# Kernel optimization log

Hardware: AMD Instinct MI355X
Metric: run time of the kernel (lower is better)

Reference implementation:

```python
import jax, jax.numpy as jnp
import numpy as np


def _lstm(x, Wih, Whh, bih, bhh):
    # x: [T,B,E] -> outputs [T,B,H]; torch gate order i,f,g,o
    B = x.shape[1]
    H = Whh.shape[1]
    bias = bih + bhh
    def step(carry, xt):
        h, c = carry
        g = xt @ Wih.T + h @ Whh.T + bias  # [B,4H]
        i, f, gg, o = jnp.split(g, 4, axis=-1)
        c = jax.nn.sigmoid(f) * c + jax.nn.sigmoid(i) * jnp.tanh(gg)
        h = jax.nn.sigmoid(o) * jnp.tanh(c)
        return (h, c), h
    init = (jnp.zeros((B, H), x.dtype), jnp.zeros((B, H), x.dtype))
    _, hs = jax.lax.scan(step, init, x)
    return hs


def setup_inputs():
    key = jax.random.key(0)
    ks = jax.random.split(key, 16)
    B, T, V, NT, E, H = 128, 512, 50000, 24, 128, 256
    Hd = H // 2  # per-direction hidden
    s = 0.08
    x = jax.random.randint(ks[0], (B, T), 0, V)
    tags = jax.random.randint(ks[1], (B, T), 0, NT)
    lengths = jax.random.randint(ks[2], (B,), T // 2, T + 1)
    mask = jnp.arange(T)[None, :] < lengths[:, None]  # [B,T] bool, position 0 always valid
    emb = (jax.random.normal(ks[3], (V, E)) * s).at[0].set(0.0)  # padding_idx=0 row zeroed
    Wih_f = jax.random.normal(ks[4], (4 * Hd, E)) * s
    Whh_f = jax.random.normal(ks[5], (4 * Hd, Hd)) * s
    bih_f = jax.random.normal(ks[6], (4 * Hd,)) * s
    bhh_f = jax.random.normal(ks[7], (4 * Hd,)) * s
    Wih_b = jax.random.normal(ks[8], (4 * Hd, E)) * s
    Whh_b = jax.random.normal(ks[9], (4 * Hd, Hd)) * s
    bih_b = jax.random.normal(ks[10], (4 * Hd,)) * s
    bhh_b = jax.random.normal(ks[11], (4 * Hd,)) * s
    W_out = jax.random.normal(ks[12], (NT, H)) * s
    b_out = jnp.zeros((NT,))
    transitions = jax.random.normal(ks[13], (NT, NT))
    start_trans = jax.random.normal(ks[14], (NT,))
    end_trans = jax.random.normal(ks[15], (NT,))
    return {"x": x, "tags": tags, "mask": mask, "emb": emb,
            "Wih_f": Wih_f, "Whh_f": Whh_f, "bih_f": bih_f, "bhh_f": bhh_f,
            "Wih_b": Wih_b, "Whh_b": Whh_b, "bih_b": bih_b, "bhh_b": bhh_b,
            "W_out": W_out, "b_out": b_out, "transitions": transitions,
            "start_trans": start_trans, "end_trans": end_trans}


def reference(x, tags, mask, emb, Wih_f, Whh_f, bih_f, bhh_f,
              Wih_b, Whh_b, bih_b, bhh_b, W_out, b_out,
              transitions, start_trans, end_trans):
    # --- emissions (dropout is identity in eval) ---
    xe = emb[x]                       # [B,T,E]
    xt = xe.transpose(1, 0, 2)        # [T,B,E]
    hf = _lstm(xt, Wih_f, Whh_f, bih_f, bhh_f)               # [T,B,Hd]
    hb = _lstm(xt[::-1], Wih_b, Whh_b, bih_b, bhh_b)[::-1]   # [T,B,Hd]
    h = jnp.concatenate([hf, hb], axis=-1).transpose(1, 0, 2)  # [B,T,H]
    emissions = h @ W_out.T + b_out   # [B,T,NT]

    # --- CRF forward algorithm (logZ) via scan over time ---
    score0 = start_trans + emissions[:, 0]  # [B,NT]
    em_rest = emissions[:, 1:].transpose(1, 0, 2)  # [T-1,B,NT]
    m_rest = mask[:, 1:].T                        # [T-1,B]
    def fwd_step(score, inp):
        em_t, m_t = inp
        ns = jax.nn.logsumexp(score[:, :, None] + transitions[None] + em_t[:, None, :], axis=1)
        return jnp.where(m_t[:, None], ns, score), None
    score, _ = jax.lax.scan(fwd_step, score0, (em_rest, m_rest))
    logZ = jax.nn.logsumexp(score + end_trans, axis=1)  # [B]

    # --- gold path score, fully vectorized ---
    mf = mask.astype(emissions.dtype)
    emit = jnp.take_along_axis(emissions, tags[:, :, None], axis=2)[:, :, 0]  # [B,T]
    trans = transitions[tags[:, :-1], tags[:, 1:]]                            # [B,T-1]
    gold = start_trans[tags[:, 0]] + emit[:, 0] + jnp.sum((trans + emit[:, 1:]) * mf[:, 1:], axis=1)
    last_idx = mask.sum(axis=1) - 1
    last_tags = jnp.take_along_axis(tags, last_idx[:, None], axis=1)[:, 0]
    gold = gold + end_trans[last_tags]

    return jnp.mean(logZ - gold)
```

## Files before the change

kernel.cpp:

```cpp
#include <hip/hip_runtime.h>
#include <hip/hip_bf16.h>

typedef unsigned short u16;
typedef unsigned int   u32;
typedef _Float16 half2_t __attribute__((ext_vector_type(2)));
typedef short    bf16x8 __attribute__((ext_vector_type(8)));
typedef float    f32x4  __attribute__((ext_vector_type(4)));
typedef u32      u32x4v __attribute__((ext_vector_type(4)));

#define TT   512

__device__ __forceinline__ float sigf(float x)  { return 1.0f / (1.0f + __expf(-x)); }
__device__ __forceinline__ float tanhf_(float x){ return 1.0f - 2.0f / (__expf(2.0f * x) + 1.0f); }

__device__ __forceinline__ u16 f2bf(float x) {
  __hip_bfloat16 h = __float2bfloat16(x);
  return *reinterpret_cast<u16*>(&h);
}
__device__ __forceinline__ float bf2f(u16 u) { return __uint_as_float(((u32)u) << 16); }
__device__ __forceinline__ u32 pk2(float a, float b) {
  return (u32)f2bf(a) | ((u32)f2bf(b) << 16);
}
__device__ __forceinline__ u16 f2h(float x) {
  _Float16 h = (_Float16)x;
  union { _Float16 f; u16 u; } c; c.f = h; return c.u;
}
__device__ __forceinline__ half2_t u2h2(u32 v) {
  union { u32 u; half2_t h; } c; c.u = v; return c.h;
}

__global__ __launch_bounds__(256) void prep_k(
    const float* __restrict__ Wih_f, const float* __restrict__ Wih_b,
    const float* __restrict__ Whh_f, const float* __restrict__ Whh_b,
    const float* __restrict__ bih_f, const float* __restrict__ bhh_f,
    const float* __restrict__ bih_b, const float* __restrict__ bhh_b,
    const float* __restrict__ W_out,
    u16* __restrict__ Wb, u32* __restrict__ Whh16, float* __restrict__ bias,
    u32* __restrict__ Wout16)
{
  int i = blockIdx.x * 256 + threadIdx.x;
  {
    int n = i >> 7, k = i & 127;
    float v = (n < 512) ? Wih_f[n * 128 + k] : Wih_b[(n - 512) * 128 + k];
    Wb[i] = f2bf(v);
  }
  if (i < 65536) {
    int d = i >> 15, rem = i & 32767, r = rem >> 6, kp = rem & 63;
    const float* W = d ? Whh_b : Whh_f;
    float f0 = W[r * 128 + 2 * kp], f1 = W[r * 128 + 2 * kp + 1];
    Whh16[i] = (u32)f2h(f0) | ((u32)f2h(f1) << 16);
  }
  if (i < 1024) {
    int d = i >> 9, jj = i & 511;
    bias[i] = d ? (bih_b[jj] + bhh_b[jj]) : (bih_f[jj] + bhh_f[jj]);
  }
  if (i < 3072) {
    Wout16[i] = (u32)f2h(W_out[2 * i]) | ((u32)f2h(W_out[2 * i + 1]) << 16);
  }
}

__global__ __launch_bounds__(256) void embed_k(
    const int* __restrict__ x, const float* __restrict__ emb, u16* __restrict__ xe)
{
  const int tid = threadIdx.x;
  const int r = blockIdx.x * 8 + (tid >> 5);
  const int lane = tid & 31;
  int token = x[r];
  float4 v = *(const float4*)&emb[(size_t)token * 128 + lane * 4];
  uint2 p; p.x = pk2(v.x, v.y); p.y = pk2(v.z, v.w);
  *(uint2*)&xe[(size_t)r * 128 + lane * 4] = p;
}

__global__ __launch_bounds__(256, 2) void gates_mfma_k(
    const u16* __restrict__ xe, const u16* __restrict__ Wb,
    const float* __restrict__ bias, u16* __restrict__ Gout)
{
  const int tid = threadIdx.x;
  const int wid = tid >> 6, l = tid & 63;
  const int wm = wid >> 1, wn = wid & 1;
  const int M0 = blockIdx.y * 128, N0 = blockIdx.x * 128;
  const int lr = l & 15, lk = l >> 4;

  f32x4 acc[4][4];
#pragma unroll
  for (int i = 0; i < 4; ++i)
#pragma unroll
    for (int j = 0; j < 4; ++j) acc[i][j] = (f32x4){0.f, 0.f, 0.f, 0.f};

#pragma unroll
  for (int ks = 0; ks < 4; ++ks) {
    bf16x8 a[4], b[4];
#pragma unroll
    for (int mi = 0; mi < 4; ++mi)
      a[mi] = *(const bf16x8*)&xe[(size_t)(M0 + wm * 64 + mi * 16 + lr) * 128 + ks * 32 + lk * 8];
#pragma unroll
    for (int ni = 0; ni < 4; ++ni)
      b[ni] = *(const bf16x8*)&Wb[(size_t)(N0 + wn * 64 + ni * 16 + lr) * 128 + ks * 32 + lk * 8];
#pragma unroll
    for (int mi = 0; mi < 4; ++mi)
#pragma unroll
      for (int ni = 0; ni < 4; ++ni)
        acc[mi][ni] = __builtin_amdgcn_mfma_f32_16x16x32_bf16(a[mi], b[ni], acc[mi][ni], 0, 0, 0);
  }

  float bcol[4];
#pragma unroll
  for (int ni = 0; ni < 4; ++ni) bcol[ni] = bias[N0 + wn * 64 + ni * 16 + lr];

  __shared__ u16 cs[128][136];
#pragma unroll
  for (int mi = 0; mi < 4; ++mi)
#pragma unroll
    for (int ni = 0; ni < 4; ++ni) {
      int col = wn * 64 + ni * 16 + lr;
#pragma unroll
      for (int r = 0; r < 4; ++r) {
        int row = wm * 64 + mi * 16 + lk * 4 + r;
        cs[row][col] = f2bf(acc[mi][ni][r] + bcol[ni]);
      }
    }
  __syncthreads();
  {
    int row = tid >> 1, c0 = (tid & 1) * 64;
    u16* dst = &Gout[(size_t)(M0 + row) * 1024 + N0 + c0];
#pragma unroll
    for (int q = 0; q < 8; ++q)
      *(uint4*)&dst[q * 8] = *(const uint4*)&cs[row][c0 + q * 8];
  }
}

__global__ __launch_bounds__(256, 1) void lstm_k(
    const u16* __restrict__ G, const u32* __restrict__ Whh16,
    u16* __restrict__ Hout)
{
  const int bid = blockIdx.x;
  const int dir = bid >> 7, b = bid & 127;
  const int tid = threadIdx.x;
  const int r   = tid & 127;
  const int hi  = tid >> 7;
  const int g0  = r + hi * 256;
  const int g1  = g0 + 128;

  const u32* w0p = Whh16 + ((size_t)dir << 15) + (size_t)g0 * 64;
  const u32* w1p = Whh16 + ((size_t)dir << 15) + (size_t)g1 * 64;

#define LDQ(n) u32x4v q##n = *(const u32x4v*)(w0p + 4*(n)); \
               u32x4v p##n = *(const u32x4v*)(w1p + 4*(n));
  LDQ(0)  LDQ(1)  LDQ(2)  LDQ(3)  LDQ(4)  LDQ(5)  LDQ(6)  LDQ(7)
  LDQ(8)  LDQ(9)  LDQ(10) LDQ(11) LDQ(12) LDQ(13) LDQ(14) LDQ(15)
#undef LDQ
#define PIN(a,b,c,d) asm volatile("" : "+v"(a), "+v"(b), "+v"(c), "+v"(d));
  PIN(q0,q1,q2,q3)   PIN(q4,q5,q6,q7)   PIN(q8,q9,q10,q11)   PIN(q12,q13,q14,q15)
  PIN(p0,p1,p2,p3)   PIN(p4,p5,p6,p7)   PIN(p8,p9,p10,p11)   PIN(p12,p13,p14,p15)
#undef PIN

  __shared__ __align__(16) u32 hs2[64];
  __shared__ float gact[512];
  if (tid < 64) hs2[tid] = 0u;
  float c = 0.0f;
  __syncthreads();

  const u16* gp = G + (size_t)b * TT * 1024 + (size_t)dir * 512;
  int t = dir ? (TT - 1) : 0;
  const int ts = dir ? -1 : 1;
  u16 gb0 = gp[(size_t)t * 1024 + g0];
  u16 gb1 = gp[(size_t)t * 1024 + g1];

  for (int step = 0; step < TT; ++step) {
    float gpre0 = bf2f(gb0), gpre1 = bf2f(gb1);
    if (step < TT - 1) {
      gb0 = gp[(size_t)(t + ts) * 1024 + g0];
      gb1 = gp[(size_t)(t + ts) * 1024 + g1];
    }

    float a00 = 0.f, a01 = 0.f, a10 = 0.f, a11 = 0.f;
    const u32x4v* h4 = (const u32x4v*)hs2;
#define DOT(n) { u32x4v hv = h4[n]; \
    a00 = __builtin_amdgcn_fdot2(u2h2(hv.x), u2h2(q##n.x), a00, false); \
    a00 = __builtin_amdgcn_fdot2(u2h2(hv.y), u2h2(q##n.y), a00, false); \
    a01 = __builtin_amdgcn_fdot2(u2h2(hv.z), u2h2(q##n.z), a01, false); \
    a01 = __builtin_amdgcn_fdot2(u2h2(hv.w), u2h2(q##n.w), a01, false); \
    a10 = __builtin_amdgcn_fdot2(u2h2(hv.x), u2h2(p##n.x), a10, false); \
    a10 = __builtin_amdgcn_fdot2(u2h2(hv.y), u2h2(p##n.y), a10, false); \
    a11 = __builtin_amdgcn_fdot2(u2h2(hv.z), u2h2(p##n.z), a11, false); \
    a11 = __builtin_amdgcn_fdot2(u2h2(hv.w), u2h2(p##n.w), a11, false); }
    DOT(0)  DOT(1)  DOT(2)  DOT(3)  DOT(4)  DOT(5)  DOT(6)  DOT(7)
    DOT(8)  DOT(9)  DOT(10) DOT(11) DOT(12) DOT(13) DOT(14) DOT(15)
#undef DOT
    float v0 = gpre0 + a00 + a01;
    float v1 = gpre1 + a10 + a11;

    float act0, act1;
    if (hi == 0) { act0 = sigf(v0);   act1 = sigf(v1); }
    else         { act0 = tanhf_(v0); act1 = sigf(v1); }
    gact[g0] = act0; gact[g1] = act1;
    __syncthreads();
    if (hi == 0) {
      float iv = gact[r], fv = gact[128 + r], gv = gact[256 + r], ov = gact[384 + r];
      c = fv * c + iv * gv;
      float hvv = ov * tanhf_(c);
      ((u16*)hs2)[r] = f2h(hvv);
      Hout[((size_t)(b * TT + t)) * 256 + dir * 128 + r] = f2h(hvv);
    }
    __syncthreads();
    t += ts;
  }
}

__global__ __launch_bounds__(256) void emis_k(
    const u16* __restrict__ Hb, const u32* __restrict__ Wout16,
    const float* __restrict__ b_out, float* __restrict__ em)
{
  __shared__ __align__(16) u32 wl2[24 * 128];
  __shared__ float bo[24];
  const int tid = threadIdx.x;
  for (int i = tid; i < 3072; i += 256) wl2[i] = Wout16[i];
  if (tid < 24) bo[tid] = b_out[tid];
  __syncthreads();

  const int m = blockIdx.x * 256 + tid;
  float acc[24];
#pragma unroll
  for (int tg = 0; tg < 24; ++tg) acc[tg] = bo[tg];

  const u32* h2 = (const u32*)(Hb + (size_t)m * 256);
  for (int ck = 0; ck < 16; ++ck) {
    uint4 hv = *(const uint4*)(h2 + ck * 4);
#pragma unroll
    for (int tg = 0; tg < 24; ++tg) {
      u32x4v wv = *(const u32x4v*)&wl2[tg * 128 + ck * 4];
      float a = acc[tg];
      a = __builtin_amdgcn_fdot2(u2h2(hv.x), u2h2(wv.x), a, false);
      a = __builtin_amdgcn_fdot2(u2h2(hv.y), u2h2(wv.y), a, false);
      a = __builtin_amdgcn_fdot2(u2h2(hv.z), u2h2(wv.z), a, false);
      a = __builtin_amdgcn_fdot2(u2h2(hv.w), u2h2(wv.w), a, false);
      acc[tg] = a;
    }
  }
#pragma unroll
  for (int t6 = 0; t6 < 6; ++t6) {
    float4 o;
    o.x = acc[t6*4+0]; o.y = acc[t6*4+1]; o.z = acc[t6*4+2]; o.w = acc[t6*4+3];
    *(float4*)&em[(size_t)m * 24 + t6 * 4] = o;
  }
}

__device__ __forceinline__ int get_mask(const void* mp, int idx, bool byte_mode) {
  return byte_mode ? (int)((const unsigned char*)mp)[idx] : ((const int*)mp)[idx];
}

__global__ __launch_bounds__(64) void crf_k(
    const float* __restrict__ em, const int* __restrict__ tags,
    const void* __restrict__ maskp, const float* __restrict__ trans,
    const float* __restrict__ start_tr, const float* __restrict__ end_tr,
    float* __restrict__ out)
{
  const int b = blockIdx.x;
  const int tid = threadIdx.x;
  __shared__ float tr[24 * 24];
  __shared__ float scs[24];
  for (int i = tid; i < 24 * 24; i += 64) tr[i] = trans[i];
  const bool byte_mode = (*(const u32*)maskp != 1u);

  int cnt = 0;
  for (int t = tid; t < TT; t += 64) cnt += get_mask(maskp, b * TT + t, byte_mode);
#pragma unroll
  for (int off = 32; off > 0; off >>= 1) cnt += __shfl_down(cnt, off);
  cnt = __shfl(cnt, 0);

  if (tid < 24) scs[tid] = start_tr[tid] + em[(size_t)(b * TT) * 24 + tid];
  __syncthreads();

  const int j = tid >> 1, h = tid & 1;
  const bool act = (tid < 48);
  float em_next = 0.f;
  if (act && h == 0 && cnt > 1) em_next = em[(size_t)(b * TT + 1) * 24 + j];

  for (int t = 1; t < cnt; ++t) {
    float em_cur = em_next;
    if (act && h == 0 && t + 1 < cnt) em_next = em[(size_t)(b * TT + t + 1) * 24 + j];
    float ns = 0.f;
    if (act) {
      const int base = h * 12;
      float vv[12];
      float mx = -1e30f;
#pragma unroll
      for (int i = 0; i < 12; ++i) {
        vv[i] = scs[base + i] + tr[(base + i) * 24 + j];
        mx = fmaxf(mx, vv[i]);
      }
      float s = 0.f;
#pragma unroll
      for (int i = 0; i < 12; ++i) s += __expf(vv[i] - mx);
      float mo = __shfl_xor(mx, 1), so = __shfl_xor(s, 1);
      float M = fmaxf(mx, mo);
      s = s * __expf(mx - M) + so * __expf(mo - M);
      ns = em_cur + M + __logf(s);
    }
    __syncthreads();
    if (act && h == 0) scs[j] = ns;
    __syncthreads();
  }

  float lzv = 0.f;
  if (tid == 0) {
    float mx = -1e30f;
    for (int i = 0; i < 24; ++i) mx = fmaxf(mx, scs[i] + end_tr[i]);
    float s = 0.f;
    for (int i = 0; i < 24; ++i) s += __expf(scs[i] + end_tr[i] - mx);
    lzv = mx + __logf(s);
  }

  float part = 0.f;
  for (int t = tid; t < TT; t += 64) {
    if (t >= 1 && t < cnt) {
      int tp = tags[b * TT + t - 1], tc = tags[b * TT + t];
      part += tr[tp * 24 + tc] + em[((size_t)(b * TT + t)) * 24 + tc];
    }
  }
#pragma unroll
  for (int off = 32; off > 0; off >>= 1) part += __shfl_down(part, off);
  if (tid == 0) {
    int t0g = tags[b * TT];
    float gold = start_tr[t0g] + em[(size_t)(b * TT) * 24 + t0g] + part;
    gold += end_tr[tags[b * TT + cnt - 1]];
    atomicAdd(out, (lzv - gold) * (1.0f / 128.0f));
  }
}

extern "C" void kernel_launch(void* const* d_in, const int* in_sizes, int n_in,
                              void* d_out, int out_size, void* d_ws, size_t ws_size,
                              hipStream_t stream) {
  const int*   x     = (const int*)d_in[0];
  const int*   tags  = (const int*)d_in[1];
  const void*  mask  = d_in[2];
  const float* emb   = (const float*)d_in[3];
  const float* Wih_f = (const float*)d_in[4];
  const float* Whh_f = (const float*)d_in[5];
  const float* bih_f = (const float*)d_in[6];
  const float* bhh_f = (const float*)d_in[7];
  const float* Wih_b = (const float*)d_in[8];
  const float* Whh_b = (const float*)d_in[9];
  const float* bih_b = (const float*)d_in[10];
  const float* bhh_b = (const float*)d_in[11];
  const float* W_out = (const float*)d_in[12];
  const float* b_out = (const float*)d_in[13];
  const float* trans = (const float*)d_in[14];
  const float* st_tr = (const float*)d_in[15];
  const float* en_tr = (const float*)d_in[16];

  u16*   Gb     = (u16*)d_ws;
  u16*   Hb     = Gb + (size_t)65536 * 1024;
  float* em     = (float*)(Hb + (size_t)65536 * 256);
  float* bias   = em + (size_t)65536 * 24;
  u16*   Wb     = (u16*)(bias + 1024);
  u32*   Whh16  = (u32*)(Wb + 131072);
  u32*   Wout16 = Whh16 + 65536;
  u16*   xe     = Hb;

  prep_k<<<512, 256, 0, stream>>>(Wih_f, Wih_b, Whh_f, Whh_b,
                                  bih_f, bhh_f, bih_b, bhh_b, W_out,
                                  Wb, Whh16, bias, Wout16);
  embed_k<<<8192, 256, 0, stream>>>(x, emb, xe);
  gates_mfma_k<<<dim3(8, 512), 256, 0, stream>>>(xe, Wb, bias, Gb);
  lstm_k<<<256, 256, 0, stream>>>(Gb, Whh16, Hb);
  emis_k<<<256, 256, 0, stream>>>(Hb, Wout16, b_out, em);
  hipMemsetAsync(d_out, 0, sizeof(float), stream);
  crf_k<<<128, 64, 0, stream>>>(em, tags, mask, trans, st_tr, en_tr, (float*)d_out);
}
```

Measured before the change: 704.9 us.

## Deepen LSTM gate prefetch and make CRF forward a barrier-free register/shuffle scan

The LSTM recurrence now prefetches gate preactivations two steps ahead instead of one, and the register-pinning asm is moved inside the loop after the dot products. This is meant to hide global load latency behind more than one step of work. The CRF kernel keeps its 12 transition values per lane in registers and exchanges scores with wave shuffles instead of shared memory. That drops the two __syncthreads per timestep and the shared-memory traffic in the serial logsumexp scan. The final logZ is computed with a wave reduction, at the cost of a few more registers and redundant shuffles.

```diff
diff --git a/kernel.cpp b/kernel.cpp
--- a/kernel.cpp
+++ b/kernel.cpp
@@ -149,10 +149,6 @@
   LDQ(0)  LDQ(1)  LDQ(2)  LDQ(3)  LDQ(4)  LDQ(5)  LDQ(6)  LDQ(7)
   LDQ(8)  LDQ(9)  LDQ(10) LDQ(11) LDQ(12) LDQ(13) LDQ(14) LDQ(15)
 #undef LDQ
-#define PIN(a,b,c,d) asm volatile("" : "+v"(a), "+v"(b), "+v"(c), "+v"(d));
-  PIN(q0,q1,q2,q3)   PIN(q4,q5,q6,q7)   PIN(q8,q9,q10,q11)   PIN(q12,q13,q14,q15)
-  PIN(p0,p1,p2,p3)   PIN(p4,p5,p6,p7)   PIN(p8,p9,p10,p11)   PIN(p12,p13,p14,p15)
-#undef PIN
 
   __shared__ __align__(16) u32 hs2[64];
   __shared__ float gact[512];
@@ -163,15 +159,18 @@
   const u16* gp = G + (size_t)b * TT * 1024 + (size_t)dir * 512;
   int t = dir ? (TT - 1) : 0;
   const int ts = dir ? -1 : 1;
-  u16 gb0 = gp[(size_t)t * 1024 + g0];
-  u16 gb1 = gp[(size_t)t * 1024 + g1];
+  u16 cur0 = gp[(size_t)t * 1024 + g0];
+  u16 cur1 = gp[(size_t)t * 1024 + g1];
+  u16 nxt0 = gp[(size_t)(t + ts) * 1024 + g0];
+  u16 nxt1 = gp[(size_t)(t + ts) * 1024 + g1];
 
   for (int step = 0; step < TT; ++step) {
-    float gpre0 = bf2f(gb0), gpre1 = bf2f(gb1);
-    if (step < TT - 1) {
-      gb0 = gp[(size_t)(t + ts) * 1024 + g0];
-      gb1 = gp[(size_t)(t + ts) * 1024 + g1];
-    }
+    u16 pf0 = 0, pf1 = 0;
+    if (step + 2 < TT) {
+      pf0 = gp[(size_t)(t + 2 * ts) * 1024 + g0];
+      pf1 = gp[(size_t)(t + 2 * ts) * 1024 + g1];
+    }
+    float gpre0 = bf2f(cur0), gpre1 = bf2f(cur1);
 
     float a00 = 0.f, a01 = 0.f, a10 = 0.f, a11 = 0.f;
     const u32x4v* h4 = (const u32x4v*)hs2;
@@ -187,6 +186,12 @@
     DOT(0)  DOT(1)  DOT(2)  DOT(3)  DOT(4)  DOT(5)  DOT(6)  DOT(7)
     DOT(8)  DOT(9)  DOT(10) DOT(11) DOT(12) DOT(13) DOT(14) DOT(15)
 #undef DOT
+
+#define PIN(a,b,c,d) asm volatile("" : "+v"(a), "+v"(b), "+v"(c), "+v"(d));
+    PIN(q0,q1,q2,q3)   PIN(q4,q5,q6,q7)   PIN(q8,q9,q10,q11)   PIN(q12,q13,q14,q15)
+    PIN(p0,p1,p2,p3)   PIN(p4,p5,p6,p7)   PIN(p8,p9,p10,p11)   PIN(p12,p13,p14,p15)
+#undef PIN
+
     float v0 = gpre0 + a00 + a01;
     float v1 = gpre1 + a10 + a11;
 
@@ -203,6 +208,7 @@
       Hout[((size_t)(b * TT + t)) * 256 + dir * 128 + r] = f2h(hvv);
     }
     __syncthreads();
+    cur0 = nxt0; cur1 = nxt1; nxt0 = pf0; nxt1 = pf1;
     t += ts;
   }
 }
@@ -257,9 +263,6 @@
 {
   const int b = blockIdx.x;
   const int tid = threadIdx.x;
-  __shared__ float tr[24 * 24];
-  __shared__ float scs[24];
-  for (int i = tid; i < 24 * 24; i += 64) tr[i] = trans[i];
   const bool byte_mode = (*(const u32*)maskp != 1u);
 
   int cnt = 0;
@@ -268,54 +271,55 @@
   for (int off = 32; off > 0; off >>= 1) cnt += __shfl_down(cnt, off);
   cnt = __shfl(cnt, 0);
 
-  if (tid < 24) scs[tid] = start_tr[tid] + em[(size_t)(b * TT) * 24 + tid];
-  __syncthreads();
-
-  const int j = tid >> 1, h = tid & 1;
   const bool act = (tid < 48);
+  const int j  = (tid < 24) ? tid : tid - 24;
+  const int i0 = (tid < 24) ? 0 : 12;
+  const int partner = (tid < 24) ? tid + 24 : tid - 24;
+
+  float tr_reg[12];
+  if (act) {
+#pragma unroll
+    for (int k = 0; k < 12; ++k) tr_reg[k] = trans[(i0 + k) * 24 + j];
+  }
+
+  float sc = 0.f;
+  if (act) sc = start_tr[j] + em[(size_t)(b * TT) * 24 + j];
   float em_next = 0.f;
-  if (act && h == 0 && cnt > 1) em_next = em[(size_t)(b * TT + 1) * 24 + j];
+  if (act && cnt > 1) em_next = em[(size_t)(b * TT + 1) * 24 + j];
 
   for (int t = 1; t < cnt; ++t) {
     float em_cur = em_next;
-    if (act && h == 0 && t + 1 < cnt) em_next = em[(size_t)(b * TT + t + 1) * 24 + j];
-    float ns = 0.f;
-    if (act) {
-      const int base = h * 12;
-      float vv[12];
-      float mx = -1e30f;
-#pragma unroll
-      for (int i = 0; i < 12; ++i) {
-        vv[i] = scs[base + i] + tr[(base + i) * 24 + j];
-        mx = fmaxf(mx, vv[i]);
-      }
-      float s = 0.f;
-#pragma unroll
-      for (int i = 0; i < 12; ++i) s += __expf(vv[i] - mx);
-      float mo = __shfl_xor(mx, 1), so = __shfl_xor(s, 1);
-      float M = fmaxf(mx, mo);
-      s = s * __expf(mx - M) + so * __expf(mo - M);
-      ns = em_cur + M + __logf(s);
-    }
-    __syncthreads();
-    if (act && h == 0) scs[j] = ns;
-    __syncthreads();
-  }
-
-  float lzv = 0.f;
-  if (tid == 0) {
-    float mx = -1e30f;
-    for (int i = 0; i < 24; ++i) mx = fmaxf(mx, scs[i] + end_tr[i]);
+    if (act && t + 1 < cnt) em_next = em[(size_t)(b * TT + t + 1) * 24 + j];
+
+    float v[12];
+#pragma unroll
+    for (int k = 0; k < 12; ++k) v[k] = __shfl(sc, i0 + k) + tr_reg[k];
+    float mx = fmaxf(fmaxf(fmaxf(v[0], v[1]), fmaxf(v[2], v[3])),
+                     fmaxf(fmaxf(v[4], v[5]), fmaxf(v[6], v[7])));
+    mx = fmaxf(mx, fmaxf(fmaxf(v[8], v[9]), fmaxf(v[10], v[11])));
     float s = 0.f;
-    for (int i = 0; i < 24; ++i) s += __expf(scs[i] + end_tr[i] - mx);
-    lzv = mx + __logf(s);
-  }
+#pragma unroll
+    for (int k = 0; k < 12; ++k) s += __expf(v[k] - mx);
+    float mo = __shfl(mx, partner), so = __shfl(s, partner);
+    float M = fmaxf(mx, mo);
+    s = s * __expf(mx - M) + so * __expf(mo - M);
+    sc = act ? (em_cur + M + __logf(s)) : 0.f;
+  }
+
+  float z = (tid < 24) ? sc + end_tr[tid] : -1e30f;
+  float zm = z;
+#pragma unroll
+  for (int off = 32; off > 0; off >>= 1) zm = fmaxf(zm, __shfl_xor(zm, off));
+  float ze = (tid < 24) ? __expf(z - zm) : 0.f;
+#pragma unroll
+  for (int off = 32; off > 0; off >>= 1) ze += __shfl_xor(ze, off);
+  float lzv = zm + __logf(ze);
 
   float part = 0.f;
   for (int t = tid; t < TT; t += 64) {
     if (t >= 1 && t < cnt) {
       int tp = tags[b * TT + t - 1], tc = tags[b * TT + t];
-      part += tr[tp * 24 + tc] + em[((size_t)(b * TT + t)) * 24 + tc];
+      part += trans[tp * 24 + tc] + em[((size_t)(b * TT + t)) * 24 + tc];
     }
   }
 #pragma unroll
```

Result: slower. 753.4 us (+6.9%).
